# Kernel optimization log

Hardware: AMD Instinct MI355X
Metric: run time of the kernel (lower is better)

Reference implementation:

```python
import jax, jax.numpy as jnp
import numpy as np
import math

B, S, D = 2, 2048, 1024
H = 16
HD = D // H
SPARSITY = 0.8


def setup_inputs() -> dict:
    key = jax.random.key(0)
    ks = jax.random.split(key, 5)
    scale = 1.0 / math.sqrt(D)
    return {
        "hidden_states": jax.random.normal(ks[0], (B, S, D), dtype=jnp.float32),
        "Wq": jax.random.normal(ks[1], (D, D), dtype=jnp.float32) * scale,
        "bq": jnp.zeros((D,), dtype=jnp.float32),
        "Wk": jax.random.normal(ks[2], (D, D), dtype=jnp.float32) * scale,
        "bk": jnp.zeros((D,), dtype=jnp.float32),
        "Wv": jax.random.normal(ks[3], (D, D), dtype=jnp.float32) * scale,
        "bv": jnp.zeros((D,), dtype=jnp.float32),
        "Wo": jax.random.normal(ks[4], (D, D), dtype=jnp.float32) * scale,
        "bo": jnp.zeros((D,), dtype=jnp.float32),
    }


def reference(hidden_states, Wq, bq, Wk, bk, Wv, bv, Wo, bo):
    b, s, d = hidden_states.shape
    # projections (torch Linear: x @ W.T + b), split heads -> [b, h, s, hd]
    def proj(W, bias):
        y = hidden_states @ W.T + bias
        return y.reshape(b, s, H, HD).transpose(0, 2, 1, 3)

    q = proj(Wq, bq)
    k = proj(Wk, bk)
    v = proj(Wv, bv)

    # scaled dot-product scores [b, h, s, s]
    attn = jnp.einsum("bhqd,bhkd->bhqk", q, k) / math.sqrt(HD)

    # top-k threshold per query row (k-th largest == sort-descending[k-1])
    kk = max(int(s * (1.0 - SPARSITY)), 1)
    thr = jax.lax.top_k(attn, kk)[0][..., kk - 1:kk]  # [b, h, s, 1]
    attn = attn + jnp.where(attn < thr, jnp.float32(-10000.0), jnp.float32(0.0))

    attn = jax.nn.softmax(attn, axis=-1)
    out = jnp.einsum("bhqk,bhkd->bhqd", attn, v)  # [b, h, s, hd]
    out = out.transpose(0, 2, 1, 3).reshape(b, s, d)
    return out @ Wo.T + bo
```

## Files before the change

### kernel.cpp

```cpp
#include <hip/hip_runtime.h>
#include <math.h>

#define S_LEN 2048
#define NH 16
#define HDIM 64
#define BATCH 2
#define BHC 32
#define KK 409
#define DMODEL 1024

typedef __attribute__((ext_vector_type(8))) short bf16x8;
typedef __attribute__((ext_vector_type(4))) float f32x4;

#define SSTR 2052
#define T_STR  40

__device__ __forceinline__ unsigned f2ord(float f) {
    unsigned u = __float_as_uint(f);
    return (u & 0x80000000u) ? ~u : (u | 0x80000000u);
}
__device__ __forceinline__ float ord2f(unsigned v) {
    unsigned u = (v & 0x80000000u) ? (v & 0x7fffffffu) : ~v;
    return __uint_as_float(u);
}
__device__ __forceinline__ unsigned short f2bf(float f) {
    unsigned u = __float_as_uint(f);
    u += 0x7fffu + ((u >> 16) & 1u);
    return (unsigned short)(u >> 16);
}
__device__ __forceinline__ float bf2f(unsigned short h) {
    return __uint_as_float(((unsigned)h) << 16);
}

__global__ __launch_bounds__(256)
void split32(const float* __restrict__ in, unsigned short* __restrict__ hi,
             unsigned short* __restrict__ lo, int n4)
{
    const int i = blockIdx.x * 256 + threadIdx.x;
    if (i < n4) {
        const float4 v = ((const float4*)in)[i];
        ushort4 h, l;
        h.x = f2bf(v.x); l.x = f2bf(v.x - bf2f(h.x));
        h.y = f2bf(v.y); l.y = f2bf(v.y - bf2f(h.y));
        h.z = f2bf(v.z); l.z = f2bf(v.z - bf2f(h.z));
        h.w = f2bf(v.w); l.w = f2bf(v.w - bf2f(h.w));
        ((ushort4*)hi)[i] = h;
        ((ushort4*)lo)[i] = l;
    }
}

__global__ __launch_bounds__(256)
void gemm_mfma(const unsigned short* __restrict__ Ah, const unsigned short* __restrict__ Al,
               const unsigned short* __restrict__ Bh, const unsigned short* __restrict__ Bl,
               const float* __restrict__ bias, void* __restrict__ out0,
               void* __restrict__ out1, int mode)
{
    __shared__ __align__(16) unsigned short sAh[128 * T_STR];
    __shared__ __align__(16) unsigned short sAl[128 * T_STR];
    __shared__ __align__(16) unsigned short sBh[64 * T_STR];
    __shared__ __align__(16) unsigned short sBl[64 * T_STR];

    const int tid  = threadIdx.x;
    const int lane = tid & 63;
    const int w    = tid >> 6;
    const int q15  = lane & 15;
    const int quad = lane >> 4;
    const int n0b = blockIdx.x * 64;
    const int m0b = blockIdx.y * 128;
    const int wm = (w >> 1) * 64;
    const int wn = (w & 1) * 32;

    const int ar0 = tid >> 2, aks0 = (tid & 3) * 8;
    const int ar1 = (tid + 256) >> 2, aks1 = aks0;
    const int br = tid >> 2, bks = (tid & 3) * 8;

    const unsigned short* gAh0 = Ah + (size_t)(m0b + ar0) * 1024 + aks0;
    const unsigned short* gAh1 = Ah + (size_t)(m0b + ar1) * 1024 + aks1;
    const unsigned short* gAl0 = Al + (size_t)(m0b + ar0) * 1024 + aks0;
    const unsigned short* gAl1 = Al + (size_t)(m0b + ar1) * 1024 + aks1;
    const unsigned short* gBh = Bh + (size_t)(n0b + br) * 1024 + bks;
    const unsigned short* gBl = Bl + (size_t)(n0b + br) * 1024 + bks;

    f32x4 acc[4][2];
#pragma unroll
    for (int mt = 0; mt < 4; ++mt)
#pragma unroll
        for (int nt = 0; nt < 2; ++nt) acc[mt][nt] = (f32x4){0.f, 0.f, 0.f, 0.f};

#pragma unroll 1
    for (int k0 = 0; k0 < 1024; k0 += 32) {
        const bf16x8 vah0 = *(const bf16x8*)(gAh0 + k0);
        const bf16x8 vah1 = *(const bf16x8*)(gAh1 + k0);
        const bf16x8 val0 = *(const bf16x8*)(gAl0 + k0);
        const bf16x8 val1 = *(const bf16x8*)(gAl1 + k0);
        const bf16x8 vbh  = *(const bf16x8*)(gBh + k0);
        const bf16x8 vbl  = *(const bf16x8*)(gBl + k0);
        __syncthreads();
        *(bf16x8*)(sAh + ar0 * T_STR + aks0) = vah0;
        *(bf16x8*)(sAh + ar1 * T_STR + aks1) = vah1;
        *(bf16x8*)(sAl + ar0 * T_STR + aks0) = val0;
        *(bf16x8*)(sAl + ar1 * T_STR + aks1) = val1;
        *(bf16x8*)(sBh + br * T_STR + bks) = vbh;
        *(bf16x8*)(sBl + br * T_STR + bks) = vbl;
        __syncthreads();

        bf16x8 fbh[2], fbl[2];
#pragma unroll
        for (int nt = 0; nt < 2; ++nt) {
            fbh[nt] = *(const bf16x8*)(sBh + (wn + nt * 16 + q15) * T_STR + quad * 8);
            fbl[nt] = *(const bf16x8*)(sBl + (wn + nt * 16 + q15) * T_STR + quad * 8);
        }
#pragma unroll
        for (int mt = 0; mt < 4; ++mt) {
            const bf16x8 fah = *(const bf16x8*)(sAh + (wm + mt * 16 + q15) * T_STR + quad * 8);
            const bf16x8 fal = *(const bf16x8*)(sAl + (wm + mt * 16 + q15) * T_STR + quad * 8);
#pragma unroll
            for (int nt = 0; nt < 2; ++nt) {
                acc[mt][nt] = __builtin_amdgcn_mfma_f32_16x16x32_bf16(fah, fbh[nt], acc[mt][nt], 0, 0, 0);
                acc[mt][nt] = __builtin_amdgcn_mfma_f32_16x16x32_bf16(fah, fbl[nt], acc[mt][nt], 0, 0, 0);
                acc[mt][nt] = __builtin_amdgcn_mfma_f32_16x16x32_bf16(fal, fbh[nt], acc[mt][nt], 0, 0, 0);
            }
        }
    }

#pragma unroll
    for (int nt = 0; nt < 2; ++nt) {
        const int n = n0b + wn + nt * 16 + q15;
        const float bv = bias[n];
#pragma unroll
        for (int mt = 0; mt < 4; ++mt) {
            const int mb = m0b + wm + mt * 16 + quad * 4;
#pragma unroll
            for (int rg = 0; rg < 4; ++rg) {
                const int m = mb + rg;
                const float o = acc[mt][nt][rg] + bv;
                if (mode == 0) {
                    ((float*)out0)[(size_t)m * 1024 + n] = o;
                } else {
                    const int b = m >> 11, s = m & 2047;
                    const int h = n >> 6, hd = n & 63;
                    const size_t base = ((size_t)((b * NH + h) * S_LEN + s)) * HDIM + hd;
                    if (mode == 3) {
                        ((unsigned short*)out0)[base] = f2bf(o);
                    } else {
                        const unsigned short oh = f2bf(o);
                        ((unsigned short*)out0)[base] = oh;
                        ((unsigned short*)out1)[base] = f2bf(o - bf2f(oh));
                    }
                }
            }
        }
    }
}

__global__ __launch_bounds__(256)
void transpose_v16(const unsigned short* __restrict__ V, unsigned short* __restrict__ Vt)
{
    __shared__ unsigned short t[64][72];
    const int tid = threadIdx.x;
    const int s0 = blockIdx.x * 64;
    const int bh = blockIdx.y;
    const unsigned short* Vb = V + (size_t)bh * S_LEN * HDIM;
#pragma unroll
    for (int i = 0; i < 4; ++i) {
        const int f = tid + i * 256;
        const int s = f >> 4;
        const int hq = (f & 15) * 4;
        const ushort4 v = *(const ushort4*)(Vb + (size_t)(s0 + s) * HDIM + hq);
        t[s][hq + 0] = v.x; t[s][hq + 1] = v.y; t[s][hq + 2] = v.z; t[s][hq + 3] = v.w;
    }
    __syncthreads();
    unsigned short* Vtb = Vt + (size_t)bh * HDIM * S_LEN;
#pragma unroll
    for (int i = 0; i < 4; ++i) {
        const int f = tid + i * 256;
        const int hd = f >> 4;
        const int sq = (f & 15) * 4;
        ushort4 v;
        v.x = t[sq + 0][hd]; v.y = t[sq + 1][hd];
        v.z = t[sq + 2][hd]; v.w = t[sq + 3][hd];
        *(ushort4*)(Vtb + (size_t)hd * S_LEN + s0 + sq) = v;
    }
}

__device__ __forceinline__ bf16x8 pack_hi8(const uint4 a0, const uint4 a1)
{
    union { unsigned u[4]; bf16x8 v; } c;
    c.u[0] = (a0.x >> 16) | (a0.y & 0xffff0000u);
    c.u[1] = (a0.z >> 16) | (a0.w & 0xffff0000u);
    c.u[2] = (a1.x >> 16) | (a1.y & 0xffff0000u);
    c.u[3] = (a1.z >> 16) | (a1.w & 0xffff0000u);
    return c.v;
}

__global__ __launch_bounds__(512, 2)
void attn_kernel(const unsigned short* __restrict__ Qh, const unsigned short* __restrict__ Ql,
                 const unsigned short* __restrict__ Kh, const unsigned short* __restrict__ Kl,
                 const unsigned short* __restrict__ Vt,
                 unsigned short* __restrict__ AOh, unsigned short* __restrict__ AOl)
{
    extern __shared__ __align__(16) char smem[];
    unsigned* S = (unsigned*)smem;
    float* Opart = (float*)smem;

    const int tid  = threadIdx.x;
    const int lane = tid & 63;
    const int w    = tid >> 6;
    const int q15  = lane & 15;
    const int quad = lane >> 4;

    const int blk = blockIdx.x;
    const int bh  = (blk & 7) * 4 + ((blk >> 3) & 3);
    const int q0  = (blk >> 5) * 16;

    const size_t qrow = ((size_t)bh * S_LEN + q0 + q15) * HDIM;
    const bf16x8 bqh0 = *(const bf16x8*)(Qh + qrow + quad * 8);
    const bf16x8 bqh1 = *(const bf16x8*)(Qh + qrow + 32 + quad * 8);
    const bf16x8 bql0 = *(const bf16x8*)(Ql + qrow + quad * 8);
    const bf16x8 bql1 = *(const bf16x8*)(Ql + qrow + 32 + quad * 8);

    const size_t kbase = (size_t)bh * S_LEN * HDIM;

#pragma unroll 4
    for (int t = 0; t < 16; ++t) {
        const int key = w * 256 + t * 16 + q15;
        const unsigned short* kh = Kh + kbase + (size_t)key * HDIM + quad * 8;
        const unsigned short* kl = Kl + kbase + (size_t)key * HDIM + quad * 8;
        const bf16x8 akh0 = *(const bf16x8*)(kh);
        const bf16x8 akh1 = *(const bf16x8*)(kh + 32);
        const bf16x8 akl0 = *(const bf16x8*)(kl);
        const bf16x8 akl1 = *(const bf16x8*)(kl + 32);
        f32x4 c = {0.f, 0.f, 0.f, 0.f};
        c = __builtin_amdgcn_mfma_f32_16x16x32_bf16(akh0, bqh0, c, 0, 0, 0);
        c = __builtin_amdgcn_mfma_f32_16x16x32_bf16(akh1, bqh1, c, 0, 0, 0);
        c = __builtin_amdgcn_mfma_f32_16x16x32_bf16(akh0, bql0, c, 0, 0, 0);
        c = __builtin_amdgcn_mfma_f32_16x16x32_bf16(akh1, bql1, c, 0, 0, 0);
        c = __builtin_amdgcn_mfma_f32_16x16x32_bf16(akl0, bqh0, c, 0, 0, 0);
        c = __builtin_amdgcn_mfma_f32_16x16x32_bf16(akl1, bqh1, c, 0, 0, 0);
        c = c * 0.125f;
        uint4 o;
        o.x = f2ord(c[0]); o.y = f2ord(c[1]); o.z = f2ord(c[2]); o.w = f2ord(c[3]);
        *(uint4*)(S + q15 * SSTR + w * 256 + t * 16 + quad * 4) = o;
    }
    __syncthreads();

    float invd[2];
    const int r0 = 2 * w;
#pragma unroll
    for (int rr = 0; rr < 2; ++rr) {
        const int r = r0 + rr;
        unsigned* R = S + r * SSTR;

        uint4 va[8];
#pragma unroll
        for (int i = 0; i < 8; ++i) va[i] = *(const uint4*)(R + i * 256 + lane * 4);

        unsigned umx = 0u;
#pragma unroll
        for (int i = 0; i < 8; ++i) {
            umx = va[i].x > umx ? va[i].x : umx;
            umx = va[i].y > umx ? va[i].y : umx;
            umx = va[i].z > umx ? va[i].z : umx;
            umx = va[i].w > umx ? va[i].w : umx;
        }
#pragma unroll
        for (int off = 32; off >= 1; off >>= 1) {
            const unsigned o = (unsigned)__shfl_xor((int)umx, off);
            umx = o > umx ? o : umx;
        }
        const float mx = ord2f(umx);

        unsigned T = 0u;
#pragma unroll 1
        for (int b = 31; b >= 0; --b) {
            const unsigned X = T | (1u << b);
            int c = 0;
#pragma unroll
            for (int i = 0; i < 8; ++i) {
                c += (va[i].x >= X) + (va[i].y >= X) + (va[i].z >= X) + (va[i].w >= X);
            }
            int cnt = 0;
#pragma unroll
            for (int bb = 0; bb < 6; ++bb)
                cnt += (int)(__builtin_popcountll(__ballot((c >> bb) & 1)) << bb);
            if (cnt >= KK) {
                T = X;
                if (cnt == KK) {
                    unsigned mn = 0xffffffffu;
#pragma unroll
                    for (int i = 0; i < 8; ++i) {
                        unsigned v;
                        v = va[i].x >= X ? va[i].x : 0xffffffffu; mn = v < mn ? v : mn;
                        v = va[i].y >= X ? va[i].y : 0xffffffffu; mn = v < mn ? v : mn;
                        v = va[i].z >= X ? va[i].z : 0xffffffffu; mn = v < mn ? v : mn;
                        v = va[i].w >= X ? va[i].w : 0xffffffffu; mn = v < mn ? v : mn;
                    }
#pragma unroll
                    for (int off = 32; off >= 1; off >>= 1) {
                        const unsigned o = (unsigned)__shfl_xor((int)mn, off);
                        mn = o < mn ? o : mn;
                    }
                    T = mn;
                    break;
                }
            }
        }

        float lsum = 0.f;
#pragma unroll
        for (int i = 0; i < 8; ++i) {
            const uint4 v = va[i];
            const float e0 = (v.x >= T) ? __expf(ord2f(v.x) - mx) : 0.f;
            const float e1 = (v.y >= T) ? __expf(ord2f(v.y) - mx) : 0.f;
            const float e2 = (v.z >= T) ? __expf(ord2f(v.z) - mx) : 0.f;
            const float e3 = (v.w >= T) ? __expf(ord2f(v.w) - mx) : 0.f;
            uint4 pw;
            pw.x = ((unsigned)f2bf(e0)) << 16;
            pw.y = ((unsigned)f2bf(e1)) << 16;
            pw.z = ((unsigned)f2bf(e2)) << 16;
            pw.w = ((unsigned)f2bf(e3)) << 16;
            *(uint4*)(R + i * 256 + lane * 4) = pw;
            lsum += e0 + e1 + e2 + e3;
        }
#pragma unroll
        for (int off = 32; off >= 1; off >>= 1) lsum += __shfl_xor(lsum, off);
        invd[rr] = 1.f / lsum;
    }
    __syncthreads();

    {
        f32x4 oacc[4];
#pragma unroll
        for (int ht = 0; ht < 4; ++ht) oacc[ht] = (f32x4){0.f, 0.f, 0.f, 0.f};
        const size_t vtb = (size_t)bh * HDIM * S_LEN;
        const unsigned* Srow = S + q15 * SSTR;
#pragma unroll 2
        for (int ks = 0; ks < 8; ++ks) {
            const int key0 = w * 256 + ks * 32 + quad * 8;
            const uint4 a0 = *(const uint4*)(Srow + key0);
            const uint4 a1 = *(const uint4*)(Srow + key0 + 4);
            const bf16x8 ap = pack_hi8(a0, a1);
#pragma unroll
            for (int ht = 0; ht < 4; ++ht) {
                const int hd = ht * 16 + q15;
                const bf16x8 bv = *(const bf16x8*)(Vt + vtb + (size_t)hd * S_LEN + key0);
                oacc[ht] = __builtin_amdgcn_mfma_f32_16x16x32_bf16(ap, bv, oacc[ht], 0, 0, 0);
            }
        }
        __syncthreads();
#pragma unroll
        for (int ht = 0; ht < 4; ++ht)
#pragma unroll
            for (int rg = 0; rg < 4; ++rg)
                Opart[w * 1024 + (quad * 4 + rg) * 64 + ht * 16 + q15] = oacc[ht][rg];
    }
    __syncthreads();

    {
        const int r1 = r0 + 1;
        float s0 = 0.f, s1 = 0.f;
#pragma unroll
        for (int ww = 0; ww < 8; ++ww) {
            s0 += Opart[ww * 1024 + r0 * 64 + lane];
            s1 += Opart[ww * 1024 + r1 * 64 + lane];
        }
        const int b = bh >> 4, h = bh & 15;
        const float o0 = s0 * invd[0];
        const float o1 = s1 * invd[1];
        const size_t i0 = ((size_t)(b * S_LEN + q0 + r0)) * DMODEL + h * HDIM + lane;
        const size_t i1 = ((size_t)(b * S_LEN + q0 + r1)) * DMODEL + h * HDIM + lane;
        const unsigned short h0 = f2bf(o0), h1 = f2bf(o1);
        AOh[i0] = h0; AOl[i0] = f2bf(o0 - bf2f(h0));
        AOh[i1] = h1; AOl[i1] = f2bf(o1 - bf2f(h1));
    }
}

extern "C" void kernel_launch(void* const* d_in, const int* in_sizes, int n_in,
                              void* d_out, int out_size, void* d_ws, size_t ws_size,
                              hipStream_t stream)
{
    const float* X  = (const float*)d_in[0];
    const float* Wq = (const float*)d_in[1];
    const float* bq = (const float*)d_in[2];
    const float* Wk = (const float*)d_in[3];
    const float* bk = (const float*)d_in[4];
    const float* Wv = (const float*)d_in[5];
    const float* bv = (const float*)d_in[6];
    const float* Wo = (const float*)d_in[7];
    const float* bo = (const float*)d_in[8];

    char* p = (char*)d_ws;
    const size_t NEL = (size_t)BHC * S_LEN * HDIM;
    unsigned short* Q16h = (unsigned short*)p; p += NEL * 2;
    unsigned short* Q16l = (unsigned short*)p; p += NEL * 2;
    unsigned short* K16h = (unsigned short*)p; p += NEL * 2;
    unsigned short* K16l = (unsigned short*)p; p += NEL * 2;
    unsigned short* Vb16 = (unsigned short*)p; p += NEL * 2;
    unsigned short* Vt16 = (unsigned short*)p; p += NEL * 2;
    unsigned short* Xh   = (unsigned short*)p; p += NEL * 2;
    unsigned short* Xl   = (unsigned short*)p; p += NEL * 2;
    unsigned short* AOh  = (unsigned short*)p; p += NEL * 2;
    unsigned short* AOl  = (unsigned short*)p; p += NEL * 2;
    unsigned short* Wqh  = (unsigned short*)p; p += DMODEL * DMODEL * 2;
    unsigned short* Wql  = (unsigned short*)p; p += DMODEL * DMODEL * 2;
    unsigned short* Wkh  = (unsigned short*)p; p += DMODEL * DMODEL * 2;
    unsigned short* Wkl  = (unsigned short*)p; p += DMODEL * DMODEL * 2;
    unsigned short* Wvh  = (unsigned short*)p; p += DMODEL * DMODEL * 2;
    unsigned short* Wvl  = (unsigned short*)p; p += DMODEL * DMODEL * 2;
    unsigned short* Woh  = (unsigned short*)p; p += DMODEL * DMODEL * 2;
    unsigned short* Wol  = (unsigned short*)p; p += DMODEL * DMODEL * 2;

    const int attn_lds = 16 * SSTR * 4;
    hipFuncSetAttribute((const void*)attn_kernel,
                        hipFuncAttributeMaxDynamicSharedMemorySize, attn_lds);

    const int X4 = (int)(NEL / 4);
    const int W4 = DMODEL * DMODEL / 4;

    split32<<<(X4 + 255) / 256, 256, 0, stream>>>(X,  Xh,  Xl,  X4);
    split32<<<(W4 + 255) / 256, 256, 0, stream>>>(Wq, Wqh, Wql, W4);
    split32<<<(W4 + 255) / 256, 256, 0, stream>>>(Wk, Wkh, Wkl, W4);
    split32<<<(W4 + 255) / 256, 256, 0, stream>>>(Wv, Wvh, Wvl, W4);
    split32<<<(W4 + 255) / 256, 256, 0, stream>>>(Wo, Woh, Wol, W4);

    const dim3 ggrid(16, 32, 1);
    gemm_mfma<<<ggrid, 256, 0, stream>>>(Xh, Xl, Wqh, Wql, bq, Q16h, Q16l, 2);
    gemm_mfma<<<ggrid, 256, 0, stream>>>(Xh, Xl, Wkh, Wkl, bk, K16h, K16l, 2);
    gemm_mfma<<<ggrid, 256, 0, stream>>>(Xh, Xl, Wvh, Wvl, bv, Vb16, nullptr, 3);
    transpose_v16<<<dim3(32, 32, 1), 256, 0, stream>>>(Vb16, Vt16);

    attn_kernel<<<4096, 512, attn_lds, stream>>>(Q16h, Q16l, K16h, K16l, Vt16, AOh, AOl);

    gemm_mfma<<<ggrid, 256, 0, stream>>>(AOh, AOl, Woh, Wol, bo, d_out, nullptr, 0);
}
```

Baseline: 938.1 us.

## Use bit-sliced transpose for per-row top-k radix threshold selection

Replaces the 32-iteration radix threshold search, which compared all 32 register values against a candidate on every step, with a bit-transposed (bit-sliced) representation. The 32 values per lane are transposed into 32 bit-planes so each step is an AND plus a popcount over a candidate mask, followed by wave-wide ballot counting. The max reduction is also rewritten as a balanced tree. The aim is to cut the ALU cost of the top-k threshold search in the softmax stage, at the cost of a fixed transpose overhead of about 80 swap operations per row and higher register pressure.

```diff
diff --git a/kernel.cpp b/kernel.cpp
--- a/kernel.cpp
+++ b/kernel.cpp
@@ -191,6 +191,153 @@
     c.u[2] = (a1.x >> 16) | (a1.y & 0xffff0000u);
     c.u[3] = (a1.z >> 16) | (a1.w & 0xffff0000u);
     return c.v;
+}
+
+#define TRP(AK, AKJ, J, M) { const unsigned _t = (((AK) >> (J)) ^ (AKJ)) & (M); \
+                             (AK) ^= _t << (J); (AKJ) ^= _t; }
+#define UMX(A, B) ((A) > (B) ? (A) : (B))
+
+#define SELSTEP(TB, BITV) { \
+    const unsigned eb = E & (TB); \
+    const int cl = __builtin_popcount(eb); \
+    int cnt = gcnt; \
+    cnt += (int)__builtin_popcountll(__ballot(cl & 1)); \
+    cnt += (int)__builtin_popcountll(__ballot(cl & 2)) << 1; \
+    cnt += (int)__builtin_popcountll(__ballot(cl & 4)) << 2; \
+    cnt += (int)__builtin_popcountll(__ballot(cl & 8)) << 3; \
+    cnt += (int)__builtin_popcountll(__ballot(cl & 16)) << 4; \
+    cnt += (int)__builtin_popcountll(__ballot(cl & 32)) << 5; \
+    if (cnt >= KK) { T |= (BITV); E = eb; if (cnt == KK) goto sel_done; } \
+    else { gcnt = cnt; E &= ~(TB); } \
+}
+
+#define MNU(U) { const unsigned _v = (U) >= T ? (U) : 0xffffffffu; mn = _v < mn ? _v : mn; }
+
+#define EXG(UA, UB, UC, UD, OFF) { \
+    const float ea = (UA) >= T ? __expf(ord2f(UA) - mx) : 0.f; \
+    const float eb_ = (UB) >= T ? __expf(ord2f(UB) - mx) : 0.f; \
+    const float ec = (UC) >= T ? __expf(ord2f(UC) - mx) : 0.f; \
+    const float ed = (UD) >= T ? __expf(ord2f(UD) - mx) : 0.f; \
+    uint4 wv; \
+    wv.x = ((unsigned)f2bf(ea)) << 16; \
+    wv.y = ((unsigned)f2bf(eb_)) << 16; \
+    wv.z = ((unsigned)f2bf(ec)) << 16; \
+    wv.w = ((unsigned)f2bf(ed)) << 16; \
+    *(uint4*)(R + (OFF) + lane * 4) = wv; \
+    lsum += ea + eb_ + ec + ed; }
+
+__device__ __forceinline__ float row_pass(unsigned* R, const int lane)
+{
+    const uint4 q0 = *(const uint4*)(R + 0 * 256 + lane * 4);
+    const uint4 q1 = *(const uint4*)(R + 1 * 256 + lane * 4);
+    const uint4 q2 = *(const uint4*)(R + 2 * 256 + lane * 4);
+    const uint4 q3 = *(const uint4*)(R + 3 * 256 + lane * 4);
+    const uint4 q4 = *(const uint4*)(R + 4 * 256 + lane * 4);
+    const uint4 q5 = *(const uint4*)(R + 5 * 256 + lane * 4);
+    const uint4 q6 = *(const uint4*)(R + 6 * 256 + lane * 4);
+    const uint4 q7 = *(const uint4*)(R + 7 * 256 + lane * 4);
+    const unsigned u0  = q0.x, u1  = q0.y, u2  = q0.z, u3  = q0.w;
+    const unsigned u4  = q1.x, u5  = q1.y, u6  = q1.z, u7  = q1.w;
+    const unsigned u8  = q2.x, u9  = q2.y, u10 = q2.z, u11 = q2.w;
+    const unsigned u12 = q3.x, u13 = q3.y, u14 = q3.z, u15 = q3.w;
+    const unsigned u16 = q4.x, u17 = q4.y, u18 = q4.z, u19 = q4.w;
+    const unsigned u20 = q5.x, u21 = q5.y, u22 = q5.z, u23 = q5.w;
+    const unsigned u24 = q6.x, u25 = q6.y, u26 = q6.z, u27 = q6.w;
+    const unsigned u28 = q7.x, u29 = q7.y, u30 = q7.z, u31 = q7.w;
+
+    const unsigned a0 = UMX(u0, u1),  a1 = UMX(u2, u3),  a2 = UMX(u4, u5),  a3 = UMX(u6, u7);
+    const unsigned a4 = UMX(u8, u9),  a5 = UMX(u10, u11), a6 = UMX(u12, u13), a7 = UMX(u14, u15);
+    const unsigned a8 = UMX(u16, u17), a9 = UMX(u18, u19), a10 = UMX(u20, u21), a11 = UMX(u22, u23);
+    const unsigned a12 = UMX(u24, u25), a13 = UMX(u26, u27), a14 = UMX(u28, u29), a15 = UMX(u30, u31);
+    const unsigned b0 = UMX(a0, a1), b1 = UMX(a2, a3), b2 = UMX(a4, a5), b3 = UMX(a6, a7);
+    const unsigned b4 = UMX(a8, a9), b5 = UMX(a10, a11), b6 = UMX(a12, a13), b7 = UMX(a14, a15);
+    const unsigned c0 = UMX(b0, b1), c1 = UMX(b2, b3), c2 = UMX(b4, b5), c3 = UMX(b6, b7);
+    unsigned umx = UMX(UMX(c0, c1), UMX(c2, c3));
+#pragma unroll
+    for (int off = 32; off >= 1; off >>= 1) {
+        const unsigned o = (unsigned)__shfl_xor((int)umx, off);
+        umx = o > umx ? o : umx;
+    }
+    const float mx = ord2f(umx);
+
+    unsigned t0 = u0,  t1 = u1,  t2 = u2,  t3 = u3,  t4 = u4,  t5 = u5,  t6 = u6,  t7 = u7;
+    unsigned t8 = u8,  t9 = u9,  t10 = u10, t11 = u11, t12 = u12, t13 = u13, t14 = u14, t15 = u15;
+    unsigned t16 = u16, t17 = u17, t18 = u18, t19 = u19, t20 = u20, t21 = u21, t22 = u22, t23 = u23;
+    unsigned t24 = u24, t25 = u25, t26 = u26, t27 = u27, t28 = u28, t29 = u29, t30 = u30, t31 = u31;
+    TRP(t0, t16, 16, 0x0000FFFFu) TRP(t1, t17, 16, 0x0000FFFFu)
+    TRP(t2, t18, 16, 0x0000FFFFu) TRP(t3, t19, 16, 0x0000FFFFu)
+    TRP(t4, t20, 16, 0x0000FFFFu) TRP(t5, t21, 16, 0x0000FFFFu)
+    TRP(t6, t22, 16, 0x0000FFFFu) TRP(t7, t23, 16, 0x0000FFFFu)
+    TRP(t8, t24, 16, 0x0000FFFFu) TRP(t9, t25, 16, 0x0000FFFFu)
+    TRP(t10, t26, 16, 0x0000FFFFu) TRP(t11, t27, 16, 0x0000FFFFu)
+    TRP(t12, t28, 16, 0x0000FFFFu) TRP(t13, t29, 16, 0x0000FFFFu)
+    TRP(t14, t30, 16, 0x0000FFFFu) TRP(t15, t31, 16, 0x0000FFFFu)
+    TRP(t0, t8, 8, 0x00FF00FFu)  TRP(t1, t9, 8, 0x00FF00FFu)
+    TRP(t2, t10, 8, 0x00FF00FFu) TRP(t3, t11, 8, 0x00FF00FFu)
+    TRP(t4, t12, 8, 0x00FF00FFu) TRP(t5, t13, 8, 0x00FF00FFu)
+    TRP(t6, t14, 8, 0x00FF00FFu) TRP(t7, t15, 8, 0x00FF00FFu)
+    TRP(t16, t24, 8, 0x00FF00FFu) TRP(t17, t25, 8, 0x00FF00FFu)
+    TRP(t18, t26, 8, 0x00FF00FFu) TRP(t19, t27, 8, 0x00FF00FFu)
+    TRP(t20, t28, 8, 0x00FF00FFu) TRP(t21, t29, 8, 0x00FF00FFu)
+    TRP(t22, t30, 8, 0x00FF00FFu) TRP(t23, t31, 8, 0x00FF00FFu)
+    TRP(t0, t4, 4, 0x0F0F0F0Fu)  TRP(t1, t5, 4, 0x0F0F0F0Fu)
+    TRP(t2, t6, 4, 0x0F0F0F0Fu)  TRP(t3, t7, 4, 0x0F0F0F0Fu)
+    TRP(t8, t12, 4, 0x0F0F0F0Fu) TRP(t9, t13, 4, 0x0F0F0F0Fu)
+    TRP(t10, t14, 4, 0x0F0F0F0Fu) TRP(t11, t15, 4, 0x0F0F0F0Fu)
+    TRP(t16, t20, 4, 0x0F0F0F0Fu) TRP(t17, t21, 4, 0x0F0F0F0Fu)
+    TRP(t18, t22, 4, 0x0F0F0F0Fu) TRP(t19, t23, 4, 0x0F0F0F0Fu)
+    TRP(t24, t28, 4, 0x0F0F0F0Fu) TRP(t25, t29, 4, 0x0F0F0F0Fu)
+    TRP(t26, t30, 4, 0x0F0F0F0Fu) TRP(t27, t31, 4, 0x0F0F0F0Fu)
+    TRP(t0, t2, 2, 0x33333333u)  TRP(t1, t3, 2, 0x33333333u)
+    TRP(t4, t6, 2, 0x33333333u)  TRP(t5, t7, 2, 0x33333333u)
+    TRP(t8, t10, 2, 0x33333333u) TRP(t9, t11, 2, 0x33333333u)
+    TRP(t12, t14, 2, 0x33333333u) TRP(t13, t15, 2, 0x33333333u)
+    TRP(t16, t18, 2, 0x33333333u) TRP(t17, t19, 2, 0x33333333u)
+    TRP(t20, t22, 2, 0x33333333u) TRP(t21, t23, 2, 0x33333333u)
+    TRP(t24, t26, 2, 0x33333333u) TRP(t25, t27, 2, 0x33333333u)
+    TRP(t28, t30, 2, 0x33333333u) TRP(t29, t31, 2, 0x33333333u)
+    TRP(t0, t1, 1, 0x55555555u)  TRP(t2, t3, 1, 0x55555555u)
+    TRP(t4, t5, 1, 0x55555555u)  TRP(t6, t7, 1, 0x55555555u)
+    TRP(t8, t9, 1, 0x55555555u)  TRP(t10, t11, 1, 0x55555555u)
+    TRP(t12, t13, 1, 0x55555555u) TRP(t14, t15, 1, 0x55555555u)
+    TRP(t16, t17, 1, 0x55555555u) TRP(t18, t19, 1, 0x55555555u)
+    TRP(t20, t21, 1, 0x55555555u) TRP(t22, t23, 1, 0x55555555u)
+    TRP(t24, t25, 1, 0x55555555u) TRP(t26, t27, 1, 0x55555555u)
+    TRP(t28, t29, 1, 0x55555555u) TRP(t30, t31, 1, 0x55555555u)
+
+    unsigned T = 0u, E = 0xffffffffu;
+    int gcnt = 0;
+    SELSTEP(t31, 1u << 31) SELSTEP(t30, 1u << 30) SELSTEP(t29, 1u << 29) SELSTEP(t28, 1u << 28)
+    SELSTEP(t27, 1u << 27) SELSTEP(t26, 1u << 26) SELSTEP(t25, 1u << 25) SELSTEP(t24, 1u << 24)
+    SELSTEP(t23, 1u << 23) SELSTEP(t22, 1u << 22) SELSTEP(t21, 1u << 21) SELSTEP(t20, 1u << 20)
+    SELSTEP(t19, 1u << 19) SELSTEP(t18, 1u << 18) SELSTEP(t17, 1u << 17) SELSTEP(t16, 1u << 16)
+    SELSTEP(t15, 1u << 15) SELSTEP(t14, 1u << 14) SELSTEP(t13, 1u << 13) SELSTEP(t12, 1u << 12)
+    SELSTEP(t11, 1u << 11) SELSTEP(t10, 1u << 10) SELSTEP(t9, 1u << 9)   SELSTEP(t8, 1u << 8)
+    SELSTEP(t7, 1u << 7)   SELSTEP(t6, 1u << 6)   SELSTEP(t5, 1u << 5)   SELSTEP(t4, 1u << 4)
+    SELSTEP(t3, 1u << 3)   SELSTEP(t2, 1u << 2)   SELSTEP(t1, 1u << 1)   SELSTEP(t0, 1u)
+sel_done: ;
+    {
+        unsigned mn = 0xffffffffu;
+        MNU(u0) MNU(u1) MNU(u2) MNU(u3) MNU(u4) MNU(u5) MNU(u6) MNU(u7)
+        MNU(u8) MNU(u9) MNU(u10) MNU(u11) MNU(u12) MNU(u13) MNU(u14) MNU(u15)
+        MNU(u16) MNU(u17) MNU(u18) MNU(u19) MNU(u20) MNU(u21) MNU(u22) MNU(u23)
+        MNU(u24) MNU(u25) MNU(u26) MNU(u27) MNU(u28) MNU(u29) MNU(u30) MNU(u31)
+#pragma unroll
+        for (int off = 32; off >= 1; off >>= 1) {
+            const unsigned o = (unsigned)__shfl_xor((int)mn, off);
+            mn = o < mn ? o : mn;
+        }
+        T = mn;
+    }
+
+    float lsum = 0.f;
+    EXG(u0, u1, u2, u3, 0 * 256)    EXG(u4, u5, u6, u7, 1 * 256)
+    EXG(u8, u9, u10, u11, 2 * 256)  EXG(u12, u13, u14, u15, 3 * 256)
+    EXG(u16, u17, u18, u19, 4 * 256) EXG(u20, u21, u22, u23, 5 * 256)
+    EXG(u24, u25, u26, u27, 6 * 256) EXG(u28, u29, u30, u31, 7 * 256)
+#pragma unroll
+    for (int off = 32; off >= 1; off >>= 1) lsum += __shfl_xor(lsum, off);
+    return 1.f / lsum;
 }
 
 __global__ __launch_bounds__(512, 2)
@@ -244,88 +391,9 @@
     }
     __syncthreads();
 
-    float invd[2];
     const int r0 = 2 * w;
-#pragma unroll
-    for (int rr = 0; rr < 2; ++rr) {
-        const int r = r0 + rr;
-        unsigned* R = S + r * SSTR;
-
-        uint4 va[8];
-#pragma unroll
-        for (int i = 0; i < 8; ++i) va[i] = *(const uint4*)(R + i * 256 + lane * 4);
-
-        unsigned umx = 0u;
-#pragma unroll
-        for (int i = 0; i < 8; ++i) {
-            umx = va[i].x > umx ? va[i].x : umx;
-            umx = va[i].y > umx ? va[i].y : umx;
-            umx = va[i].z > umx ? va[i].z : umx;
-            umx = va[i].w > umx ? va[i].w : umx;
-        }
-#pragma unroll
-        for (int off = 32; off >= 1; off >>= 1) {
-            const unsigned o = (unsigned)__shfl_xor((int)umx, off);
-            umx = o > umx ? o : umx;
-        }
-        const float mx = ord2f(umx);
-
-        unsigned T = 0u;
-#pragma unroll 1
-        for (int b = 31; b >= 0; --b) {
-            const unsigned X = T | (1u << b);
-            int c = 0;
-#pragma unroll
-            for (int i = 0; i < 8; ++i) {
-                c += (va[i].x >= X) + (va[i].y >= X) + (va[i].z >= X) + (va[i].w >= X);
-            }
-            int cnt = 0;
-#pragma unroll
-            for (int bb = 0; bb < 6; ++bb)
-                cnt += (int)(__builtin_popcountll(__ballot((c >> bb) & 1)) << bb);
-            if (cnt >= KK) {
-                T = X;
-                if (cnt == KK) {
-                    unsigned mn = 0xffffffffu;
-#pragma unroll
-                    for (int i = 0; i < 8; ++i) {
-                        unsigned v;
-                        v = va[i].x >= X ? va[i].x : 0xffffffffu; mn = v < mn ? v : mn;
-                        v = va[i].y >= X ? va[i].y : 0xffffffffu; mn = v < mn ? v : mn;
-                        v = va[i].z >= X ? va[i].z : 0xffffffffu; mn = v < mn ? v : mn;
-                        v = va[i].w >= X ? va[i].w : 0xffffffffu; mn = v < mn ? v : mn;
-                    }
-#pragma unroll
-                    for (int off = 32; off >= 1; off >>= 1) {
-                        const unsigned o = (unsigned)__shfl_xor((int)mn, off);
-                        mn = o < mn ? o : mn;
-                    }
-                    T = mn;
-                    break;
-                }
-            }
-        }
-
-        float lsum = 0.f;
-#pragma unroll
-        for (int i = 0; i < 8; ++i) {
-            const uint4 v = va[i];
-            const float e0 = (v.x >= T) ? __expf(ord2f(v.x) - mx) : 0.f;
-            const float e1 = (v.y >= T) ? __expf(ord2f(v.y) - mx) : 0.f;
-            const float e2 = (v.z >= T) ? __expf(ord2f(v.z) - mx) : 0.f;
-            const float e3 = (v.w >= T) ? __expf(ord2f(v.w) - mx) : 0.f;
-            uint4 pw;
-            pw.x = ((unsigned)f2bf(e0)) << 16;
-            pw.y = ((unsigned)f2bf(e1)) << 16;
-            pw.z = ((unsigned)f2bf(e2)) << 16;
-            pw.w = ((unsigned)f2bf(e3)) << 16;
-            *(uint4*)(R + i * 256 + lane * 4) = pw;
-            lsum += e0 + e1 + e2 + e3;
-        }
-#pragma unroll
-        for (int off = 32; off >= 1; off >>= 1) lsum += __shfl_xor(lsum, off);
-        invd[rr] = 1.f / lsum;
-    }
+    const float invd0 = row_pass(S + r0 * SSTR, lane);
+    const float invd1 = row_pass(S + (r0 + 1) * SSTR, lane);
     __syncthreads();
 
     {
@@ -365,8 +433,8 @@
             s1 += Opart[ww * 1024 + r1 * 64 + lane];
         }
         const int b = bh >> 4, h = bh & 15;
-        const float o0 = s0 * invd[0];
-        const float o1 = s1 * invd[1];
+        const float o0 = s0 * invd0;
+        const float o1 = s1 * invd1;
         const size_t i0 = ((size_t)(b * S_LEN + q0 + r0)) * DMODEL + h * HDIM + lane;
         const size_t i1 = ((size_t)(b * S_LEN + q0 + r1)) * DMODEL + h * HDIM + lane;
         const unsigned short h0 = f2bf(o0), h1 = f2bf(o1);
```

New measurement: 815.1 us. -13.1%, faster.
